# Performance work log

Hardware: AMD Instinct MI355X
Metric: run time of the kernel (lower is better)

Reference implementation:

```python
import jax, jax.numpy as jnp
import numpy as np

DIM = 1024
NUM_HEADS = 16
HEAD_DIM = DIM // NUM_HEADS
EPS = 1e-6


def layer_norm(x, gamma, beta):
    # normalize over last dim (head_dim)
    mu = jnp.mean(x, axis=-1, keepdims=True)
    var = jnp.mean(jnp.square(x - mu), axis=-1, keepdims=True)
    return (x - mu) / jnp.sqrt(var + EPS) * gamma + beta


def apply_rope(q, k):
    # q, k: [B, S, H, D]; computed in fp32 (attn_fp32=True)
    seq_len, head_dim = q.shape[1], q.shape[3]
    half = head_dim // 2
    freq_range = jnp.arange(half, dtype=jnp.float32) / half
    inv_freq = 1.0 / (10000.0 ** freq_range)                       # [half]
    t = jnp.arange(seq_len, dtype=jnp.float32)                     # [S]
    freqs = jnp.outer(t, inv_freq)                                 # [S, half]
    emb = jnp.concatenate([freqs, freqs], axis=-1)                 # [S, D]
    cos = jnp.cos(emb)[None, :, None, :]                           # [1, S, 1, D]
    sin = jnp.sin(emb)[None, :, None, :]

    def rotate_half(x):
        x1, x2 = x[..., :half], x[..., half:]
        return jnp.concatenate([-x2, x1], axis=-1)

    return q * cos + rotate_half(q) * sin, k * cos + rotate_half(k) * sin


def setup_inputs() -> dict:
    key = jax.random.key(0)
    ks = jax.random.split(key, 4)
    B, S = 2, 2048
    x = jax.random.normal(ks[0], (B, S, DIM), dtype=jnp.float32)
    # xavier-uniform-ish scale for linear weights (torch Linear layout: [out, in])
    lim_qkv = float(np.sqrt(6.0 / (DIM + 3 * DIM)))
    w_qkv = jax.random.uniform(ks[1], (3 * DIM, DIM), dtype=jnp.float32, minval=-lim_qkv, maxval=lim_qkv)
    lim_p = float(np.sqrt(6.0 / (DIM + DIM)))
    w_proj = jax.random.uniform(ks[2], (DIM, DIM), dtype=jnp.float32, minval=-lim_p, maxval=lim_p)
    b_proj = jnp.zeros((DIM,), dtype=jnp.float32)
    q_gamma = jnp.ones((HEAD_DIM,), dtype=jnp.float32)
    q_beta = jnp.zeros((HEAD_DIM,), dtype=jnp.float32)
    k_gamma = jnp.ones((HEAD_DIM,), dtype=jnp.float32)
    k_beta = jnp.zeros((HEAD_DIM,), dtype=jnp.float32)
    return {"x": x, "w_qkv": w_qkv, "w_proj": w_proj, "b_proj": b_proj,
            "q_gamma": q_gamma, "q_beta": q_beta, "k_gamma": k_gamma, "k_beta": k_beta}


def reference(x, w_qkv, w_proj, b_proj, q_gamma, q_beta, k_gamma, k_beta):
    B, S, C = x.shape
    H, D = NUM_HEADS, HEAD_DIM
    qkv = jnp.einsum('bsc,oc->bso', x, w_qkv).reshape(B, S, 3, H, D)
    q = layer_norm(qkv[:, :, 0], q_gamma, q_beta)   # [B, S, H, D]
    k = layer_norm(qkv[:, :, 1], k_gamma, k_beta)
    v = qkv[:, :, 2]
    q, k = apply_rope(q, k)
    # attn_fp32=True: scores in fp32
    scale = D ** (-0.5)
    q = q.astype(jnp.float32) * scale
    k = k.astype(jnp.float32)
    v = v.astype(jnp.float32)
    attn = jnp.einsum('bqhd,bkhd->bhqk', q, k)      # [B, H, S, S]
    attn = jax.nn.softmax(attn, axis=-1)
    out = jnp.einsum('bhqk,bkhd->bqhd', attn, v).reshape(B, S, C)
    out = jnp.einsum('bsc,oc->bso', out, w_proj) + b_proj
    return out
```

## Files before the change

kernel.cpp:

```cpp
#include <hip/hip_runtime.h>
#include <math.h>

#define DIM   1024
#define NH    16
#define HD    64
#define BATCH 2
#define SEQ   2048
#define EPS   1e-6f

#define NX  (BATCH * SEQ * DIM)
#define NWQ (3 * DIM * DIM)
#define NWP (DIM * DIM)

typedef __attribute__((ext_vector_type(8))) short bf16x8;
typedef __attribute__((ext_vector_type(4))) float f32x4;

#define EXP2F(x) __builtin_amdgcn_exp2f(x)
#define LOG2E 1.4426950408889634f
#define SOFTMAX_SHIFT 12.0f

__device__ __forceinline__ float bf2f(unsigned short u) {
  return __uint_as_float(((unsigned int)u) << 16);
}
__device__ __forceinline__ unsigned short f2bf(float f) {
  unsigned int u = __float_as_uint(f);
  unsigned int r = (u + 0x7FFFu + ((u >> 16) & 1u)) >> 16;
  return (unsigned short)r;
}
__device__ __forceinline__ unsigned int pack_bf16_trunc(float p0, float p1) {
  return (__float_as_uint(p1) & 0xFFFF0000u) | (__float_as_uint(p0) >> 16);
}

__device__ __forceinline__ void async_copy16(const void* g, void* l) {
  __builtin_amdgcn_global_load_lds(
      (const __attribute__((address_space(1))) unsigned int*)g,
      (__attribute__((address_space(3))) unsigned int*)l, 16, 0, 0);
}


__global__ void detect_dtype(const unsigned short* __restrict__ w, int* __restrict__ flag) {
  __shared__ int cnt;
  if (threadIdx.x == 0) cnt = 0;
  __syncthreads();
  int c = 0;
  for (int i = threadIdx.x; i < 4096; i += 256) {
    unsigned short u = w[i];
    if ((u & 0x7F80u) >= 0x3F80u) ++c;
  }
  atomicAdd(&cnt, c);
  __syncthreads();
  if (threadIdx.x == 0) *flag = (cnt >= 64) ? 1 : 0;
}

__global__ __launch_bounds__(256)
void rope_table(float2* __restrict__ tab) {
  const int idx = blockIdx.x * 256 + threadIdx.x;
  const int s = idx >> 5, f = idx & 31;
  const float invf = expf(-((float)f * (1.f / 32.f)) * 9.210340371976184f);
  float sn, cs;
  sincosf((float)s * invf, &sn, &cs);
  tab[idx] = make_float2(cs, sn);
}

__global__ __launch_bounds__(256)
void convert_all(const void* __restrict__ x, const void* __restrict__ wq,
                 const void* __restrict__ wp,
                 unsigned short* __restrict__ xb, unsigned short* __restrict__ wqb,
                 unsigned short* __restrict__ wpb, const int* __restrict__ flagp) {
  const bool isf32 = (*flagp != 0);
  int i = (blockIdx.x * 256 + threadIdx.x) * 8;
  const void* src;
  unsigned short* dst;
  if (i < NX) { src = x; dst = xb; }
  else if (i < NX + NWQ) { src = wq; dst = wqb; i -= NX; }
  else if (i < NX + NWQ + NWP) { src = wp; dst = wpb; i -= NX + NWQ; }
  else return;
  if (isf32) {
    const float* s = (const float*)src + i;
    float4 a = *(const float4*)s;
    float4 b = *(const float4*)(s + 4);
    ushort4 lo, hi;
    lo.x = f2bf(a.x); lo.y = f2bf(a.y); lo.z = f2bf(a.z); lo.w = f2bf(a.w);
    hi.x = f2bf(b.x); hi.y = f2bf(b.y); hi.z = f2bf(b.z); hi.w = f2bf(b.w);
    *(ushort4*)&dst[i] = lo;
    *(ushort4*)&dst[i + 4] = hi;
  } else {
    *(uint4*)&dst[i] = *(const uint4*)((const unsigned short*)src + i);
  }
}

__device__ __forceinline__ float ld_param(const void* p, bool isf32, int idx) {
  return isf32 ? ((const float*)p)[idx] : bf2f(((const unsigned short*)p)[idx]);
}

__global__ __launch_bounds__(256)
void gemm_qkv(const unsigned short* __restrict__ A, const unsigned short* __restrict__ B,
              unsigned short* __restrict__ Qb, unsigned short* __restrict__ Kb,
              unsigned short* __restrict__ VbT,
              const void* __restrict__ qg, const void* __restrict__ qbe,
              const void* __restrict__ kg, const void* __restrict__ kbe,
              const float2* __restrict__ tab, const int* __restrict__ flagp) {
  __shared__ __attribute__((aligned(16))) unsigned short As[2][128 * 32];
  __shared__ __attribute__((aligned(16))) unsigned short Bs[2][128 * 32];

  const int K = DIM;
  const int tid  = threadIdx.x;
  const int wv   = tid >> 6;
  const int lane = tid & 63;
  const int l15  = lane & 15;
  const int quad = lane >> 4;
  const int wm = wv >> 1, wn = wv & 1;
  const int bm = blockIdx.y * 128;
  const int bn = blockIdx.x * 128;
  const int qsw = (quad ^ ((l15 >> 1) & 3)) * 8;

  f32x4 acc[4][4];
#pragma unroll
  for (int i = 0; i < 4; ++i)
#pragma unroll
    for (int j = 0; j < 4; ++j) acc[i][j] = (f32x4){0.f, 0.f, 0.f, 0.f};

  const int srow = tid >> 2;
  const int kseg = (((tid & 3) ^ ((tid >> 3) & 3))) * 8;
  const unsigned short* Ag = A + (size_t)(bm + srow) * K + kseg;
  const unsigned short* Bg = B + (size_t)(bn + srow) * K + kseg;

  async_copy16(Ag, &As[0][wv * 512]);
  async_copy16(Ag + (size_t)64 * K, &As[0][wv * 512 + 2048]);
  async_copy16(Bg, &Bs[0][wv * 512]);
  async_copy16(Bg + (size_t)64 * K, &Bs[0][wv * 512 + 2048]);
  __syncthreads();

  for (int k0 = 0; k0 < K; k0 += 32) {
    const int cur = (k0 >> 5) & 1, nxt = cur ^ 1;
    if (k0 + 32 < K) {
      async_copy16(Ag + k0 + 32, &As[nxt][wv * 512]);
      async_copy16(Ag + (size_t)64 * K + k0 + 32, &As[nxt][wv * 512 + 2048]);
      async_copy16(Bg + k0 + 32, &Bs[nxt][wv * 512]);
      async_copy16(Bg + (size_t)64 * K + k0 + 32, &Bs[nxt][wv * 512 + 2048]);
    }

    bf16x8 af[4], bf[4];
#pragma unroll
    for (int mt = 0; mt < 4; ++mt)
      af[mt] = *(const bf16x8*)&As[cur][(wm * 64 + mt * 16 + l15) * 32 + qsw];
#pragma unroll
    for (int nt = 0; nt < 4; ++nt)
      bf[nt] = *(const bf16x8*)&Bs[cur][(wn * 64 + nt * 16 + l15) * 32 + qsw];
#pragma unroll
    for (int mt = 0; mt < 4; ++mt)
#pragma unroll
      for (int nt = 0; nt < 4; ++nt)
        acc[mt][nt] = __builtin_amdgcn_mfma_f32_16x16x32_bf16(af[mt], bf[nt], acc[mt][nt], 0, 0, 0);
    __syncthreads();
  }

  const bool isf32 = (*flagp != 0);
  const int type = bn >> 10;
  const int h = ((bn & 1023) >> 6) + wn;

  if (type == 2) {
#pragma unroll
    for (int mt = 0; mt < 4; ++mt) {
      const int r0 = bm + wm * 64 + mt * 16 + quad * 4;
      const int b = r0 >> 11, s0 = r0 & 2047;
#pragma unroll
      for (int nt = 0; nt < 4; ++nt) {
        const int d = nt * 16 + l15;
        uint2 pk;
        pk.x = ((unsigned int)f2bf(acc[mt][nt][1]) << 16) | f2bf(acc[mt][nt][0]);
        pk.y = ((unsigned int)f2bf(acc[mt][nt][3]) << 16) | f2bf(acc[mt][nt][2]);
        *(uint2*)&VbT[((size_t)(b * NH + h) * HD + d) * SEQ + s0] = pk;
      }
    }
    return;
  }

  unsigned short* plane = (type == 0) ? Qb : Kb;
  const void* gp = (type == 0) ? qg : kg;
  const void* bp = (type == 0) ? qbe : kbe;
  float gam[4], bet[4];
#pragma unroll
  for (int nt = 0; nt < 4; ++nt) {
    gam[nt] = ld_param(gp, isf32, nt * 16 + l15);
    bet[nt] = ld_param(bp, isf32, nt * 16 + l15);
  }
  const float scale = (type == 0) ? (0.125f * LOG2E) : 1.f;

#pragma unroll
  for (int mt = 0; mt < 4; ++mt)
#pragma unroll
    for (int rr = 0; rr < 4; ++rr) {
      const int r = bm + wm * 64 + mt * 16 + quad * 4 + rr;
      const int b = r >> 11, s = r & 2047;
      float sum = acc[mt][0][rr] + acc[mt][1][rr] + acc[mt][2][rr] + acc[mt][3][rr];
      sum += __shfl_xor(sum, 1); sum += __shfl_xor(sum, 2);
      sum += __shfl_xor(sum, 4); sum += __shfl_xor(sum, 8);
      const float mu = sum * (1.f / 64.f);
      float vs = 0.f;
#pragma unroll
      for (int nt = 0; nt < 4; ++nt) {
        const float d = acc[mt][nt][rr] - mu;
        vs += d * d;
      }
      vs += __shfl_xor(vs, 1); vs += __shfl_xor(vs, 2);
      vs += __shfl_xor(vs, 4); vs += __shfl_xor(vs, 8);
      const float rs = rsqrtf(vs * (1.f / 64.f) + EPS);
      float xn[4];
#pragma unroll
      for (int nt = 0; nt < 4; ++nt)
        xn[nt] = (acc[mt][nt][rr] - mu) * rs * gam[nt] + bet[nt];
      const float2 t0 = tab[s * 32 + l15];
      const float2 t1 = tab[s * 32 + 16 + l15];
      float ro[4];
      ro[0] = xn[0] * t0.x - xn[2] * t0.y;
      ro[2] = xn[2] * t0.x + xn[0] * t0.y;
      ro[1] = xn[1] * t1.x - xn[3] * t1.y;
      ro[3] = xn[3] * t1.x + xn[1] * t1.y;
      unsigned short* row = plane + (((size_t)(b * NH + h) * SEQ + s) * HD);
#pragma unroll
      for (int nt = 0; nt < 4; ++nt)
        row[nt * 16 + l15] = f2bf(ro[nt] * scale);
    }
}

#define KIDX(g,k0,key,dim) (((((g)*2+(k0))*64+(key))*32)+(dim))
#define VOFF 8192
#define POFF 16384
#define PIDX(w,row,col) (POFF + ((w)*32+(row))*72 + (col))

__global__ __launch_bounds__(512, 4)
void attn_mfma5(const unsigned short* __restrict__ Qb, const unsigned short* __restrict__ Kb,
                const unsigned short* __restrict__ VbT, unsigned short* __restrict__ O) {
  __shared__ __attribute__((aligned(16))) unsigned short SMEM[34816];

  const int tid  = threadIdx.x;
  const int wv   = tid >> 6;
  const int g    = wv >> 2;
  const int qsub = wv & 3;
  const int lane = tid & 63;
  const int l15  = lane & 15;
  const int quad = lane >> 4;
  const int bh = blockIdx.y;
  const int q0 = blockIdx.x * 128;
  const size_t base  = (size_t)bh * (SEQ * HD);
  const size_t baseT = (size_t)bh * (HD * SEQ);
  const int qsw = (quad ^ ((l15 >> 1) & 3)) * 8;

  bf16x8 qf[2][2];
#pragma unroll
  for (int mt = 0; mt < 2; ++mt)
#pragma unroll
    for (int k0 = 0; k0 < 2; ++k0)
      qf[mt][k0] = *(const bf16x8*)&Qb[base + (size_t)(q0 + qsub * 32 + mt * 16 + l15) * HD + k0 * 32 + quad * 8];

  bf16x8 ones;
#pragma unroll
  for (int j = 0; j < 8; ++j) ones[j] = (short)0x3F80;

  f32x4 oaccT[4][2];
  f32x4 ol[2];
#pragma unroll
  for (int nb = 0; nb < 4; ++nb)
#pragma unroll
    for (int mt = 0; mt < 2; ++mt) oaccT[nb][mt] = (f32x4){0.f, 0.f, 0.f, 0.f};
  ol[0] = (f32x4){0.f, 0.f, 0.f, 0.f};
  ol[1] = (f32x4){0.f, 0.f, 0.f, 0.f};

  const int sseg = (((lane & 3) ^ ((lane >> 3) & 3))) * 8;
  const unsigned short* srcK = Kb + base + (size_t)(qsub * 16 + (lane >> 2)) * HD + sseg;
  const unsigned short* srcV = VbT + baseT + (size_t)(qsub * 16 + (lane >> 2)) * SEQ + sseg;
  unsigned short* dstK0 = &SMEM[KIDX(g, 0, qsub * 16, 0)];
  unsigned short* dstK1 = &SMEM[KIDX(g, 1, qsub * 16, 0)];
  unsigned short* dstV0 = &SMEM[VOFF + KIDX(g, 0, qsub * 16, 0)];
  unsigned short* dstV1 = &SMEM[VOFF + KIDX(g, 1, qsub * 16, 0)];

  for (int it = 0; it < SEQ / 128; ++it) {
    const int kt = it * 128 + g * 64;
    __syncthreads();
    async_copy16(srcK + (size_t)kt * HD,      dstK0);
    async_copy16(srcK + (size_t)kt * HD + 32, dstK1);
    async_copy16(srcV + kt,                   dstV0);
    async_copy16(srcV + kt + 32,              dstV1);
    __syncthreads();

    f32x4 st[4][2];
#pragma unroll
    for (int nb = 0; nb < 4; ++nb)
#pragma unroll
      for (int mt = 0; mt < 2; ++mt) st[nb][mt] = (f32x4){0.f, 0.f, 0.f, 0.f};
#pragma unroll
    for (int k0 = 0; k0 < 2; ++k0)
#pragma unroll
      for (int nb = 0; nb < 4; ++nb) {
        bf16x8 kf = *(const bf16x8*)&SMEM[KIDX(g, k0, nb * 16 + l15, qsw)];
#pragma unroll
        for (int mt = 0; mt < 2; ++mt)
          st[nb][mt] = __builtin_amdgcn_mfma_f32_16x16x32_bf16(kf, qf[mt][k0], st[nb][mt], 0, 0, 0);
      }

#pragma unroll
    for (int mt = 0; mt < 2; ++mt)
#pragma unroll
      for (int nb = 0; nb < 4; ++nb) {
        const float p0 = EXP2F(st[nb][mt][0] - SOFTMAX_SHIFT);
        const float p1 = EXP2F(st[nb][mt][1] - SOFTMAX_SHIFT);
        const float p2 = EXP2F(st[nb][mt][2] - SOFTMAX_SHIFT);
        const float p3 = EXP2F(st[nb][mt][3] - SOFTMAX_SHIFT);
        uint2 pk;
        pk.x = pack_bf16_trunc(p0, p1);
        pk.y = pack_bf16_trunc(p2, p3);
        *(uint2*)&SMEM[PIDX(wv, mt * 16 + l15, nb * 16 + quad * 4)] = pk;
      }

#pragma unroll
    for (int k0 = 0; k0 < 2; ++k0) {
      bf16x8 pf0 = *(const bf16x8*)&SMEM[PIDX(wv, 0 * 16 + l15, k0 * 32 + quad * 8)];
      bf16x8 pf1 = *(const bf16x8*)&SMEM[PIDX(wv, 1 * 16 + l15, k0 * 32 + quad * 8)];
      ol[0] = __builtin_amdgcn_mfma_f32_16x16x32_bf16(ones, pf0, ol[0], 0, 0, 0);
      ol[1] = __builtin_amdgcn_mfma_f32_16x16x32_bf16(ones, pf1, ol[1], 0, 0, 0);
#pragma unroll
      for (int nb = 0; nb < 4; ++nb) {
        bf16x8 vf = *(const bf16x8*)&SMEM[VOFF + KIDX(g, k0, nb * 16 + l15, qsw)];
        oaccT[nb][0] = __builtin_amdgcn_mfma_f32_16x16x32_bf16(vf, pf0, oaccT[nb][0], 0, 0, 0);
        oaccT[nb][1] = __builtin_amdgcn_mfma_f32_16x16x32_bf16(vf, pf1, oaccT[nb][1], 0, 0, 0);
      }
    }
  }

  __syncthreads();
  f32x4* MO = (f32x4*)SMEM;
  float* ML = (float*)(SMEM + POFF);
  if (g == 1) {
#pragma unroll
    for (int mt = 0; mt < 2; ++mt) {
#pragma unroll
      for (int nb = 0; nb < 4; ++nb)
        MO[(((qsub * 2 + mt) * 4 + nb) << 6) + lane] = oaccT[nb][mt];
      if (quad == 0)
        ML[(qsub * 2 + mt) * 16 + l15] = ol[mt][0];
    }
  }
  __syncthreads();
  if (g == 0) {
    const int b = bh >> 4, h = bh & 15;
#pragma unroll
    for (int mt = 0; mt < 2; ++mt) {
      const float l1 = ML[(qsub * 2 + mt) * 16 + l15];
      const float inv = 1.f / (ol[mt][0] + l1);
      const int qrow = q0 + qsub * 32 + mt * 16 + l15;
      unsigned short* orow = O + ((size_t)(b * SEQ + qrow)) * DIM + h * HD;
#pragma unroll
      for (int nb = 0; nb < 4; ++nb) {
        f32x4 o1 = MO[(((qsub * 2 + mt) * 4 + nb) << 6) + lane];
        uint2 pk;
        pk.x = ((unsigned int)f2bf((oaccT[nb][mt][1] + o1[1]) * inv) << 16) |
               f2bf((oaccT[nb][mt][0] + o1[0]) * inv);
        pk.y = ((unsigned int)f2bf((oaccT[nb][mt][3] + o1[3]) * inv) << 16) |
               f2bf((oaccT[nb][mt][2] + o1[2]) * inv);
        *(uint2*)&orow[nb * 16 + quad * 4] = pk;
      }
    }
  }
}

__global__ __launch_bounds__(256)
void gemm_out(const unsigned short* __restrict__ A, const unsigned short* __restrict__ B,
              const void* __restrict__ biasv, void* __restrict__ Cv,
              int M, int N, int K, const int* __restrict__ flagp) {
  __shared__ __attribute__((aligned(16))) unsigned short As[2][128 * 32];
  __shared__ __attribute__((aligned(16))) unsigned short Bs[2][64 * 32];

  const int tid  = threadIdx.x;
  const int wv   = tid >> 6;
  const int lane = tid & 63;
  const int l15  = lane & 15;
  const int quad = lane >> 4;
  const int wm = wv >> 1, wn = wv & 1;
  const int bm = blockIdx.y * 128;
  const int bn = blockIdx.x * 64;
  const int qsw = (quad ^ ((l15 >> 1) & 3)) * 8;

  f32x4 acc[4][2];
#pragma unroll
  for (int i = 0; i < 4; ++i)
#pragma unroll
    for (int j = 0; j < 2; ++j) acc[i][j] = (f32x4){0.f, 0.f, 0.f, 0.f};

  const int srow = tid >> 2;
  const int kseg = (((tid & 3) ^ ((tid >> 3) & 3))) * 8;
  const unsigned short* Ag = A + (size_t)(bm + srow) * K + kseg;
  const unsigned short* Bg = B + (size_t)(bn + srow) * K + kseg;

  async_copy16(Ag, &As[0][wv * 512]);
  async_copy16(Ag + (size_t)64 * K, &As[0][wv * 512 + 2048]);
  async_copy16(Bg, &Bs[0][wv * 512]);
  __syncthreads();

  for (int k0 = 0; k0 < K; k0 += 32) {
    const int cur = (k0 >> 5) & 1, nxt = cur ^ 1;
    if (k0 + 32 < K) {
      async_copy16(Ag + k0 + 32, &As[nxt][wv * 512]);
      async_copy16(Ag + (size_t)64 * K + k0 + 32, &As[nxt][wv * 512 + 2048]);
      async_copy16(Bg + k0 + 32, &Bs[nxt][wv * 512]);
    }

    bf16x8 af[4], bf[2];
#pragma unroll
    for (int mt = 0; mt < 4; ++mt)
      af[mt] = *(const bf16x8*)&As[cur][(wm * 64 + mt * 16 + l15) * 32 + qsw];
#pragma unroll
    for (int nt = 0; nt < 2; ++nt)
      bf[nt] = *(const bf16x8*)&Bs[cur][(wn * 32 + nt * 16 + l15) * 32 + qsw];
#pragma unroll
    for (int mt = 0; mt < 4; ++mt)
#pragma unroll
      for (int nt = 0; nt < 2; ++nt)
        acc[mt][nt] = __builtin_amdgcn_mfma_f32_16x16x32_bf16(af[mt], bf[nt], acc[mt][nt], 0, 0, 0);
    __syncthreads();
  }

  const bool isf32 = (*flagp != 0);
#pragma unroll
  for (int mt = 0; mt < 4; ++mt)
#pragma unroll
    for (int rr = 0; rr < 4; ++rr) {
      const int r = bm + wm * 64 + mt * 16 + quad * 4 + rr;
#pragma unroll
      for (int nt = 0; nt < 2; ++nt) {
        const int c = bn + wn * 32 + nt * 16 + l15;
        const float bias_c = isf32 ? ((const float*)biasv)[c]
                                   : bf2f(((const unsigned short*)biasv)[c]);
        const float o = acc[mt][nt][rr] + bias_c;
        if (isf32) ((float*)Cv)[(size_t)r * N + c] = o;
        else       ((unsigned short*)Cv)[(size_t)r * N + c] = f2bf(o);
      }
    }
}

extern "C" void kernel_launch(void* const* d_in, const int* in_sizes, int n_in,
                              void* d_out, int out_size, void* d_ws, size_t ws_size,
                              hipStream_t stream) {
  const void* x      = d_in[0];
  const void* w_qkv  = d_in[1];
  const void* w_proj = d_in[2];
  const void* b_proj = d_in[3];
  const void* q_g    = d_in[4];
  const void* q_b    = d_in[5];
  const void* k_g    = d_in[6];
  const void* k_b    = d_in[7];

  const size_t PLANE = (size_t)BATCH * NH * SEQ * HD;

  unsigned short* Qb  = (unsigned short*)d_ws;
  unsigned short* Kb  = Qb + PLANE;
  unsigned short* VbT = Kb + PLANE;
  unsigned short* xb  = VbT + PLANE;
  unsigned short* wqb = xb + PLANE;
  unsigned short* wpb = wqb + NWQ;
  float2* tab = (float2*)(wpb + NWP);
  int* flag = (int*)(tab + SEQ * 32);

  hipLaunchKernelGGL(detect_dtype, dim3(1), dim3(256), 0, stream,
                     (const unsigned short*)w_qkv, flag);
  hipLaunchKernelGGL(rope_table, dim3(SEQ * 32 / 256), dim3(256), 0, stream, tab);
  hipLaunchKernelGGL(convert_all, dim3((NX + NWQ + NWP) / 8 / 256), dim3(256), 0, stream,
                     x, w_qkv, w_proj, xb, wqb, wpb, flag);

  {
    dim3 grid((3 * DIM) / 128, (BATCH * SEQ) / 128);
    hipLaunchKernelGGL(gemm_qkv, grid, dim3(256), 0, stream,
                       xb, wqb, Qb, Kb, VbT, q_g, q_b, k_g, k_b, tab, flag);
  }
  {
    dim3 grid(SEQ / 128, BATCH * NH);
    hipLaunchKernelGGL(attn_mfma5, grid, dim3(512), 0, stream,
                       Qb, Kb, VbT, xb);
  }
  {
    dim3 grid(DIM / 64, (BATCH * SEQ) / 128);
    hipLaunchKernelGGL(gemm_out, grid, dim3(256), 0, stream,
                       xb, wpb, b_proj, d_out, BATCH * SEQ, DIM, DIM, flag);
  }
}
```

Baseline: 220.9 us.

## Load GEMM fragments directly from global memory into registers, dropping LDS staging

```diff
diff --git a/kernel.cpp b/kernel.cpp
--- a/kernel.cpp
+++ b/kernel.cpp
@@ -36,7 +36,6 @@
       (const __attribute__((address_space(1))) unsigned int*)g,
       (__attribute__((address_space(3))) unsigned int*)l, 16, 0, 0);
 }
-
 
 __global__ void detect_dtype(const unsigned short* __restrict__ w, int* __restrict__ flag) {
   __shared__ int cnt;
@@ -100,9 +99,6 @@
               const void* __restrict__ qg, const void* __restrict__ qbe,
               const void* __restrict__ kg, const void* __restrict__ kbe,
               const float2* __restrict__ tab, const int* __restrict__ flagp) {
-  __shared__ __attribute__((aligned(16))) unsigned short As[2][128 * 32];
-  __shared__ __attribute__((aligned(16))) unsigned short Bs[2][128 * 32];
-
   const int K = DIM;
   const int tid  = threadIdx.x;
   const int wv   = tid >> 6;
@@ -112,7 +108,6 @@
   const int wm = wv >> 1, wn = wv & 1;
   const int bm = blockIdx.y * 128;
   const int bn = blockIdx.x * 128;
-  const int qsw = (quad ^ ((l15 >> 1) & 3)) * 8;
 
   f32x4 acc[4][4];
 #pragma unroll
@@ -120,39 +115,44 @@
 #pragma unroll
     for (int j = 0; j < 4; ++j) acc[i][j] = (f32x4){0.f, 0.f, 0.f, 0.f};
 
-  const int srow = tid >> 2;
-  const int kseg = (((tid & 3) ^ ((tid >> 3) & 3))) * 8;
-  const unsigned short* Ag = A + (size_t)(bm + srow) * K + kseg;
-  const unsigned short* Bg = B + (size_t)(bn + srow) * K + kseg;
-
-  async_copy16(Ag, &As[0][wv * 512]);
-  async_copy16(Ag + (size_t)64 * K, &As[0][wv * 512 + 2048]);
-  async_copy16(Bg, &Bs[0][wv * 512]);
-  async_copy16(Bg + (size_t)64 * K, &Bs[0][wv * 512 + 2048]);
-  __syncthreads();
-
-  for (int k0 = 0; k0 < K; k0 += 32) {
-    const int cur = (k0 >> 5) & 1, nxt = cur ^ 1;
-    if (k0 + 32 < K) {
-      async_copy16(Ag + k0 + 32, &As[nxt][wv * 512]);
-      async_copy16(Ag + (size_t)64 * K + k0 + 32, &As[nxt][wv * 512 + 2048]);
-      async_copy16(Bg + k0 + 32, &Bs[nxt][wv * 512]);
-      async_copy16(Bg + (size_t)64 * K + k0 + 32, &Bs[nxt][wv * 512 + 2048]);
-    }
-
-    bf16x8 af[4], bf[4];
+  const unsigned short* Ab[4];
+  const unsigned short* Bb[4];
+#pragma unroll
+  for (int mt = 0; mt < 4; ++mt)
+    Ab[mt] = A + (size_t)(bm + wm * 64 + mt * 16 + l15) * K + quad * 8;
+#pragma unroll
+  for (int nt = 0; nt < 4; ++nt)
+    Bb[nt] = B + (size_t)(bn + wn * 64 + nt * 16 + l15) * K + quad * 8;
+
+  bf16x8 a0[4], b0[4];
+#pragma unroll
+  for (int mt = 0; mt < 4; ++mt) a0[mt] = *(const bf16x8*)(Ab[mt]);
+#pragma unroll
+  for (int nt = 0; nt < 4; ++nt) b0[nt] = *(const bf16x8*)(Bb[nt]);
+
+#pragma unroll
+  for (int k0 = 0; k0 < DIM; k0 += 64) {
+    bf16x8 a1[4], b1[4];
+#pragma unroll
+    for (int mt = 0; mt < 4; ++mt) a1[mt] = *(const bf16x8*)(Ab[mt] + k0 + 32);
+#pragma unroll
+    for (int nt = 0; nt < 4; ++nt) b1[nt] = *(const bf16x8*)(Bb[nt] + k0 + 32);
 #pragma unroll
     for (int mt = 0; mt < 4; ++mt)
-      af[mt] = *(const bf16x8*)&As[cur][(wm * 64 + mt * 16 + l15) * 32 + qsw];
-#pragma unroll
-    for (int nt = 0; nt < 4; ++nt)
-      bf[nt] = *(const bf16x8*)&Bs[cur][(wn * 64 + nt * 16 + l15) * 32 + qsw];
+#pragma unroll
+      for (int nt = 0; nt < 4; ++nt)
+        acc[mt][nt] = __builtin_amdgcn_mfma_f32_16x16x32_bf16(a0[mt], b0[nt], acc[mt][nt], 0, 0, 0);
+    if (k0 + 64 < DIM) {
+#pragma unroll
+      for (int mt = 0; mt < 4; ++mt) a0[mt] = *(const bf16x8*)(Ab[mt] + k0 + 64);
+#pragma unroll
+      for (int nt = 0; nt < 4; ++nt) b0[nt] = *(const bf16x8*)(Bb[nt] + k0 + 64);
+    }
 #pragma unroll
     for (int mt = 0; mt < 4; ++mt)
 #pragma unroll
       for (int nt = 0; nt < 4; ++nt)
-        acc[mt][nt] = __builtin_amdgcn_mfma_f32_16x16x32_bf16(af[mt], bf[nt], acc[mt][nt], 0, 0, 0);
-    __syncthreads();
+        acc[mt][nt] = __builtin_amdgcn_mfma_f32_16x16x32_bf16(a1[mt], b1[nt], acc[mt][nt], 0, 0, 0);
   }
 
   const bool isf32 = (*flagp != 0);
@@ -368,9 +368,6 @@
 void gemm_out(const unsigned short* __restrict__ A, const unsigned short* __restrict__ B,
               const void* __restrict__ biasv, void* __restrict__ Cv,
               int M, int N, int K, const int* __restrict__ flagp) {
-  __shared__ __attribute__((aligned(16))) unsigned short As[2][128 * 32];
-  __shared__ __attribute__((aligned(16))) unsigned short Bs[2][64 * 32];
-
   const int tid  = threadIdx.x;
   const int wv   = tid >> 6;
   const int lane = tid & 63;
@@ -379,7 +376,6 @@
   const int wm = wv >> 1, wn = wv & 1;
   const int bm = blockIdx.y * 128;
   const int bn = blockIdx.x * 64;
-  const int qsw = (quad ^ ((l15 >> 1) & 3)) * 8;
 
   f32x4 acc[4][2];
 #pragma unroll
@@ -387,37 +383,44 @@
 #pragma unroll
     for (int j = 0; j < 2; ++j) acc[i][j] = (f32x4){0.f, 0.f, 0.f, 0.f};
 
-  const int srow = tid >> 2;
-  const int kseg = (((tid & 3) ^ ((tid >> 3) & 3))) * 8;
-  const unsigned short* Ag = A + (size_t)(bm + srow) * K + kseg;
-  const unsigned short* Bg = B + (size_t)(bn + srow) * K + kseg;
-
-  async_copy16(Ag, &As[0][wv * 512]);
-  async_copy16(Ag + (size_t)64 * K, &As[0][wv * 512 + 2048]);
-  async_copy16(Bg, &Bs[0][wv * 512]);
-  __syncthreads();
-
-  for (int k0 = 0; k0 < K; k0 += 32) {
-    const int cur = (k0 >> 5) & 1, nxt = cur ^ 1;
-    if (k0 + 32 < K) {
-      async_copy16(Ag + k0 + 32, &As[nxt][wv * 512]);
-      async_copy16(Ag + (size_t)64 * K + k0 + 32, &As[nxt][wv * 512 + 2048]);
-      async_copy16(Bg + k0 + 32, &Bs[nxt][wv * 512]);
-    }
-
-    bf16x8 af[4], bf[2];
+  const unsigned short* Ab[4];
+  const unsigned short* Bb[2];
+#pragma unroll
+  for (int mt = 0; mt < 4; ++mt)
+    Ab[mt] = A + (size_t)(bm + wm * 64 + mt * 16 + l15) * K + quad * 8;
+#pragma unroll
+  for (int nt = 0; nt < 2; ++nt)
+    Bb[nt] = B + (size_t)(bn + wn * 32 + nt * 16 + l15) * K + quad * 8;
+
+  bf16x8 a0[4], b0[2];
+#pragma unroll
+  for (int mt = 0; mt < 4; ++mt) a0[mt] = *(const bf16x8*)(Ab[mt]);
+#pragma unroll
+  for (int nt = 0; nt < 2; ++nt) b0[nt] = *(const bf16x8*)(Bb[nt]);
+
+#pragma unroll
+  for (int k0 = 0; k0 < DIM; k0 += 64) {
+    bf16x8 a1[4], b1[2];
+#pragma unroll
+    for (int mt = 0; mt < 4; ++mt) a1[mt] = *(const bf16x8*)(Ab[mt] + k0 + 32);
+#pragma unroll
+    for (int nt = 0; nt < 2; ++nt) b1[nt] = *(const bf16x8*)(Bb[nt] + k0 + 32);
 #pragma unroll
     for (int mt = 0; mt < 4; ++mt)
-      af[mt] = *(const bf16x8*)&As[cur][(wm * 64 + mt * 16 + l15) * 32 + qsw];
-#pragma unroll
-    for (int nt = 0; nt < 2; ++nt)
-      bf[nt] = *(const bf16x8*)&Bs[cur][(wn * 32 + nt * 16 + l15) * 32 + qsw];
+#pragma unroll
+      for (int nt = 0; nt < 2; ++nt)
+        acc[mt][nt] = __builtin_amdgcn_mfma_f32_16x16x32_bf16(a0[mt], b0[nt], acc[mt][nt], 0, 0, 0);
+    if (k0 + 64 < DIM) {
+#pragma unroll
+      for (int mt = 0; mt < 4; ++mt) a0[mt] = *(const bf16x8*)(Ab[mt] + k0 + 64);
+#pragma unroll
+      for (int nt = 0; nt < 2; ++nt) b0[nt] = *(const bf16x8*)(Bb[nt] + k0 + 64);
+    }
 #pragma unroll
     for (int mt = 0; mt < 4; ++mt)
 #pragma unroll
       for (int nt = 0; nt < 2; ++nt)
-        acc[mt][nt] = __builtin_amdgcn_mfma_f32_16x16x32_bf16(af[mt], bf[nt], acc[mt][nt], 0, 0, 0);
-    __syncthreads();
+        acc[mt][nt] = __builtin_amdgcn_mfma_f32_16x16x32_bf16(a1[mt], b1[nt], acc[mt][nt], 0, 0, 0);
   }
 
   const bool isf32 = (*flagp != 0);
```

Result: slower. 289.8 us (+31.2%).
